# Performance work log

Measured on AMD Instinct MI355X. Metric: run time of the kernel, lower is better.

The kernel has to match this reference:

```python
import jax, jax.numpy as jnp
import numpy as np

NB_CLASSES = 8192
SZ_EMBED = 64
SMOOTHING = 0.1


def setup_inputs() -> dict:
    key = jax.random.key(0)
    k1, k2, k3 = jax.random.split(key, 3)
    X = jax.random.normal(k1, (8192, SZ_EMBED), dtype=jnp.float32)
    T = jax.random.randint(k2, (8192,), 0, NB_CLASSES)
    proxies = jax.random.normal(k3, (NB_CLASSES, SZ_EMBED), dtype=jnp.float32) / 8.0
    return {"X": X, "T": T, "proxies": proxies}


def reference(X, T, proxies):
    # L2-normalize and scale by 3 (as in the torch module)
    Xn = 3.0 * X / jnp.linalg.norm(X, axis=-1, keepdims=True)   # [N, E]
    Pn = 3.0 * proxies / jnp.linalg.norm(proxies, axis=-1, keepdims=True)  # [C, E]

    # squared pairwise distances D[i, c] = ||Xn_i - Pn_c||^2, computed once
    x_sq = jnp.sum(Xn * Xn, axis=-1, keepdims=True)             # [N, 1]
    p_sq = jnp.sum(Pn * Pn, axis=-1)                            # [C]
    D = x_sq + p_sq[None, :] - 2.0 * jnp.einsum('ne,ce->nc', Xn, Pn)  # [N, C]

    # out[i, c] = log( exp(D[i, c]) / sum_c' exp(D[i, c']) )
    out = D - jax.nn.logsumexp(D, axis=-1, keepdims=True)       # [N, C]

    # binarize + smooth labels
    nb_classes = proxies.shape[0]
    onehot = T[:, None] == jnp.arange(nb_classes)[None, :]      # [N, C] bool
    Tm = jnp.where(onehot, 1.0 - SMOOTHING, SMOOTHING / (nb_classes - 1)).astype(X.dtype)

    loss = jnp.mean(jnp.sum(-Tm * out, axis=-1))
    return loss
```

## Files before the change

kernel.cpp:

```cpp
#include <hip/hip_runtime.h>
#include <math.h>

#define NR 8192
#define NC 8192
#define EE 64
#define LOG2E   1.4426950408889634f
#define KSCALE  (-2.0f * LOG2E)
#define C18     (18.0f * LOG2E)
#define NSPLIT  32
#define CPS     (NC / NSPLIT)

typedef __attribute__((ext_vector_type(8))) short bf16x8;
typedef __attribute__((ext_vector_type(4))) float f32x4;

__device__ __forceinline__ float bf2f(unsigned short u) {
    unsigned int x = ((unsigned int)u) << 16;
    return __builtin_bit_cast(float, x);
}
__device__ __forceinline__ unsigned short f2bf(float f) {
    unsigned int u = __builtin_bit_cast(unsigned int, f);
    u += 0x7FFFu + ((u >> 16) & 1u);
    return (unsigned short)(u >> 16);
}

__global__ __launch_bounds__(256) void norm_kernel(
    const float* __restrict__ X, const float* __restrict__ P,
    unsigned short* __restrict__ Xb, unsigned short* __restrict__ Xs,
    unsigned short* __restrict__ Pb)
{
    int row  = blockIdx.x * 4 + (threadIdx.x >> 6);
    int lane = threadIdx.x & 63;
    bool isX = row < NR;
    int r = isX ? row : row - NR;
    const float* src = isX ? X : P;
    float v = src[(size_t)r * EE + lane];
    float s = v * v;
    #pragma unroll
    for (int off = 32; off; off >>= 1) s += __shfl_xor(s, off);
    float xn = v * (3.0f * rsqrtf(s));
    if (isX) {
        Xb[(size_t)r * EE + lane] = f2bf(xn);
        Xs[(size_t)r * EE + lane] = f2bf(xn * KSCALE);
    } else {
        Pb[(size_t)r * EE + lane] = f2bf(xn);
    }
}

__global__ __launch_bounds__(256) void colsum_kernel(
    const unsigned short* __restrict__ Pb, float* __restrict__ sumPnPart)
{
    int w = threadIdx.x >> 6, l = threadIdx.x & 63;
    float acc = 0.f;
    int rbase = blockIdx.x * 128 + w * 32;
    for (int i = 0; i < 32; ++i)
        acc += bf2f(Pb[(size_t)(rbase + i) * EE + l]);
    __shared__ float red[4][64];
    red[w][l] = acc;
    __syncthreads();
    if (w == 0)
        sumPnPart[blockIdx.x * 64 + l] =
            red[0][l] + red[1][l] + red[2][l] + red[3][l];
}

__global__ __launch_bounds__(256) void main_kernel(
    const unsigned short* __restrict__ Xs, const unsigned short* __restrict__ Pb,
    float* __restrict__ ePart)
{
    const int tid = threadIdx.x;
    const int w  = tid >> 6, l = tid & 63;
    const int lr = l & 15, lg = l >> 4;
    const int r0 = blockIdx.x * 256 + w * 64;
    const int cbase = blockIdx.y * CPS;
    const int s = blockIdx.y;

    bf16x8 a[4][2];
    #pragma unroll
    for (int rt = 0; rt < 4; ++rt)
        #pragma unroll
        for (int kk = 0; kk < 2; ++kk)
            a[rt][kk] = *reinterpret_cast<const bf16x8*>(
                Xs + (size_t)(r0 + rt * 16 + lr) * EE + kk * 32 + lg * 8);

    float accE[4][4] = {};
    const f32x4 dinit = {C18, C18, C18, C18};

    #pragma unroll 2
    for (int j = 0; j < CPS / 16; ++j) {
        const int c0 = cbase + j * 16;
        const size_t bb = (size_t)(c0 + lr) * EE + lg * 8;
        bf16x8 b0 = *reinterpret_cast<const bf16x8*>(Pb + bb);
        bf16x8 b1 = *reinterpret_cast<const bf16x8*>(Pb + bb + 32);
        #pragma unroll
        for (int rt = 0; rt < 4; ++rt) {
            f32x4 d = dinit;
            d = __builtin_amdgcn_mfma_f32_16x16x32_bf16(a[rt][0], b0, d, 0, 0, 0);
            d = __builtin_amdgcn_mfma_f32_16x16x32_bf16(a[rt][1], b1, d, 0, 0, 0);
            #pragma unroll
            for (int q = 0; q < 4; ++q)
                accE[rt][q] += __builtin_exp2f(d[q]);
        }
    }

    #pragma unroll
    for (int rt = 0; rt < 4; ++rt)
        #pragma unroll
        for (int q = 0; q < 4; ++q) {
            float v = accE[rt][q];
            v += __shfl_xor(v, 1);
            v += __shfl_xor(v, 2);
            v += __shfl_xor(v, 4);
            v += __shfl_xor(v, 8);
            if (lr == 0)
                ePart[(size_t)(r0 + rt * 16 + lg * 4 + q) * NSPLIT + s] = v;
        }
}

__global__ __launch_bounds__(1024) void final_kernel(
    const unsigned short* __restrict__ Xb, const unsigned short* __restrict__ Pb,
    const int* __restrict__ T, const float* __restrict__ sumPnPart,
    const float* __restrict__ ePart, float* __restrict__ lossPart)
{
    __shared__ float spn[64];
    __shared__ float terms[16];
    int wid = threadIdx.x >> 6, lane = threadIdx.x & 63;

    if (threadIdx.x < 64) {
        float s = 0.f;
        for (int b = 0; b < 64; ++b) s += sumPnPart[b * 64 + threadIdx.x];
        spn[threadIdx.x] = s;
    }
    __syncthreads();

    float sp = spn[lane];
    float wsum = 0.f;
    #pragma unroll
    for (int rr = 0; rr < 4; ++rr) {
        int row = blockIdx.x * 64 + wid * 4 + rr;
        int t = T[row];
        float x  = bf2f(Xb[(size_t)row * EE + lane]);
        float pt = bf2f(Pb[(size_t)t  * EE + lane]);
        float d1 = x * pt;
        float d2 = x * sp;
        float es = (lane < NSPLIT) ? ePart[(size_t)row * NSPLIT + lane] : 0.f;
        #pragma unroll
        for (int off = 32; off; off >>= 1) {
            d1 += __shfl_xor(d1, off);
            d2 += __shfl_xor(d2, off);
            es += __shfl_xor(es, off);
        }
        if (lane == 0) {
            float Dt   = 18.0f - 2.0f * d1;
            float sumD = (float)NC * 18.0f - 2.0f * d2;
            float lse  = __logf(es);
            wsum += lse - (0.9f * Dt + (0.1f / 8191.0f) * (sumD - Dt));
        }
    }
    if (lane == 0) terms[wid] = wsum;
    __syncthreads();
    if (threadIdx.x == 0) {
        float s = 0.f;
        #pragma unroll
        for (int i = 0; i < 16; ++i) s += terms[i];
        lossPart[blockIdx.x] = s;
    }
}

__global__ __launch_bounds__(128) void reduce_kernel(
    const float* __restrict__ lossPart, float* __restrict__ out)
{
    __shared__ float red[2];
    int w = threadIdx.x >> 6, l = threadIdx.x & 63;
    float v = lossPart[threadIdx.x];
    #pragma unroll
    for (int off = 32; off; off >>= 1) v += __shfl_xor(v, off);
    if (l == 0) red[w] = v;
    __syncthreads();
    if (threadIdx.x == 0)
        out[0] = (red[0] + red[1]) * (1.0f / (float)NR);
}

extern "C" void kernel_launch(void* const* d_in, const int* in_sizes, int n_in,
                              void* d_out, int out_size, void* d_ws, size_t ws_size,
                              hipStream_t stream)
{
    const float* X = (const float*)d_in[0];
    const int*   T = (const int*)d_in[1];
    const float* P = (const float*)d_in[2];

    unsigned short* Xb = (unsigned short*)d_ws;
    unsigned short* Xs = Xb + (size_t)NR * EE;
    unsigned short* Pb = Xs + (size_t)NR * EE;
    float* ePart     = (float*)(Pb + (size_t)NC * EE);
    float* sumPnPart = ePart + (size_t)NR * NSPLIT;
    float* lossPart  = sumPnPart + 64 * 64;
    float* out       = (float*)d_out;

    norm_kernel<<<(NR + NC) / 4, 256, 0, stream>>>(X, P, Xb, Xs, Pb);
    colsum_kernel<<<64, 256, 0, stream>>>(Pb, sumPnPart);
    main_kernel<<<dim3(NR / 256, NSPLIT), 256, 0, stream>>>(Xs, Pb, ePart);
    final_kernel<<<NR / 64, 1024, 0, stream>>>(Xb, Pb, T, sumPnPart, ePart, lossPart);
    reduce_kernel<<<1, 128, 0, stream>>>(lossPart, out);
}
```

Baseline: 47.96 us.

## Fold row-sum of distances into main kernel and fuse final reduction via ticket

The main MFMA loop now also accumulates the raw log2-scaled distances alongside the exp sums, so the separate proxy column-sum kernel and the Xb buffer are dropped. The final kernel recovers the sum of distances and target distance from the scaled Xs values. The last block reduces the per-block losses itself, using an atomic ticket that the norm kernel resets, which removes the standalone reduce launch. Two kernel launches and one workspace write are removed. The cost is extra adds in the hot loop and the bf16-scaled Xs being used for the target dot product.

```diff
diff --git a/kernel.cpp b/kernel.cpp
--- a/kernel.cpp
+++ b/kernel.cpp
@@ -5,6 +5,7 @@
 #define NC 8192
 #define EE 64
 #define LOG2E   1.4426950408889634f
+#define LN2     0.6931471805599453f
 #define KSCALE  (-2.0f * LOG2E)
 #define C18     (18.0f * LOG2E)
 #define NSPLIT  32
@@ -25,9 +26,10 @@
 
 __global__ __launch_bounds__(256) void norm_kernel(
     const float* __restrict__ X, const float* __restrict__ P,
-    unsigned short* __restrict__ Xb, unsigned short* __restrict__ Xs,
-    unsigned short* __restrict__ Pb)
+    unsigned short* __restrict__ Xs, unsigned short* __restrict__ Pb,
+    int* __restrict__ ticket)
 {
+    if (blockIdx.x == 0 && threadIdx.x == 0) *ticket = 0;
     int row  = blockIdx.x * 4 + (threadIdx.x >> 6);
     int lane = threadIdx.x & 63;
     bool isX = row < NR;
@@ -38,33 +40,15 @@
     #pragma unroll
     for (int off = 32; off; off >>= 1) s += __shfl_xor(s, off);
     float xn = v * (3.0f * rsqrtf(s));
-    if (isX) {
-        Xb[(size_t)r * EE + lane] = f2bf(xn);
+    if (isX)
         Xs[(size_t)r * EE + lane] = f2bf(xn * KSCALE);
-    } else {
+    else
         Pb[(size_t)r * EE + lane] = f2bf(xn);
-    }
-}
-
-__global__ __launch_bounds__(256) void colsum_kernel(
-    const unsigned short* __restrict__ Pb, float* __restrict__ sumPnPart)
-{
-    int w = threadIdx.x >> 6, l = threadIdx.x & 63;
-    float acc = 0.f;
-    int rbase = blockIdx.x * 128 + w * 32;
-    for (int i = 0; i < 32; ++i)
-        acc += bf2f(Pb[(size_t)(rbase + i) * EE + l]);
-    __shared__ float red[4][64];
-    red[w][l] = acc;
-    __syncthreads();
-    if (w == 0)
-        sumPnPart[blockIdx.x * 64 + l] =
-            red[0][l] + red[1][l] + red[2][l] + red[3][l];
 }
 
 __global__ __launch_bounds__(256) void main_kernel(
     const unsigned short* __restrict__ Xs, const unsigned short* __restrict__ Pb,
-    float* __restrict__ ePart)
+    float* __restrict__ part)
 {
     const int tid = threadIdx.x;
     const int w  = tid >> 6, l = tid & 63;
@@ -82,6 +66,7 @@
                 Xs + (size_t)(r0 + rt * 16 + lr) * EE + kk * 32 + lg * 8);
 
     float accE[4][4] = {};
+    float accD[4][4] = {};
     const f32x4 dinit = {C18, C18, C18, C18};
 
     #pragma unroll 2
@@ -96,8 +81,10 @@
             d = __builtin_amdgcn_mfma_f32_16x16x32_bf16(a[rt][0], b0, d, 0, 0, 0);
             d = __builtin_amdgcn_mfma_f32_16x16x32_bf16(a[rt][1], b1, d, 0, 0, 0);
             #pragma unroll
-            for (int q = 0; q < 4; ++q)
+            for (int q = 0; q < 4; ++q) {
                 accE[rt][q] += __builtin_exp2f(d[q]);
+                accD[rt][q] += d[q];
+            }
         }
     }
 
@@ -105,52 +92,52 @@
     for (int rt = 0; rt < 4; ++rt)
         #pragma unroll
         for (int q = 0; q < 4; ++q) {
-            float v = accE[rt][q];
-            v += __shfl_xor(v, 1);
-            v += __shfl_xor(v, 2);
-            v += __shfl_xor(v, 4);
-            v += __shfl_xor(v, 8);
-            if (lr == 0)
-                ePart[(size_t)(r0 + rt * 16 + lg * 4 + q) * NSPLIT + s] = v;
+            float ve = accE[rt][q];
+            float vd = accD[rt][q];
+            ve += __shfl_xor(ve, 1);  vd += __shfl_xor(vd, 1);
+            ve += __shfl_xor(ve, 2);  vd += __shfl_xor(vd, 2);
+            ve += __shfl_xor(ve, 4);  vd += __shfl_xor(vd, 4);
+            ve += __shfl_xor(ve, 8);  vd += __shfl_xor(vd, 8);
+            if (lr == 0) {
+                const size_t row = r0 + rt * 16 + lg * 4 + q;
+                part[row * 64 + s]      = ve;
+                part[row * 64 + 32 + s] = vd;
+            }
         }
 }
 
 __global__ __launch_bounds__(1024) void final_kernel(
-    const unsigned short* __restrict__ Xb, const unsigned short* __restrict__ Pb,
-    const int* __restrict__ T, const float* __restrict__ sumPnPart,
-    const float* __restrict__ ePart, float* __restrict__ lossPart)
+    const unsigned short* __restrict__ Xs, const unsigned short* __restrict__ Pb,
+    const int* __restrict__ T, const float* __restrict__ part,
+    float* __restrict__ lossPart, int* __restrict__ ticket,
+    float* __restrict__ out)
 {
-    __shared__ float spn[64];
     __shared__ float terms[16];
+    __shared__ int   isLast;
+    __shared__ float red2[2];
     int wid = threadIdx.x >> 6, lane = threadIdx.x & 63;
 
-    if (threadIdx.x < 64) {
-        float s = 0.f;
-        for (int b = 0; b < 64; ++b) s += sumPnPart[b * 64 + threadIdx.x];
-        spn[threadIdx.x] = s;
-    }
-    __syncthreads();
-
-    float sp = spn[lane];
     float wsum = 0.f;
     #pragma unroll
     for (int rr = 0; rr < 4; ++rr) {
         int row = blockIdx.x * 64 + wid * 4 + rr;
         int t = T[row];
-        float x  = bf2f(Xb[(size_t)row * EE + lane]);
+        float xs = bf2f(Xs[(size_t)row * EE + lane]);
         float pt = bf2f(Pb[(size_t)t  * EE + lane]);
-        float d1 = x * pt;
-        float d2 = x * sp;
-        float es = (lane < NSPLIT) ? ePart[(size_t)row * NSPLIT + lane] : 0.f;
+        float d1 = xs * pt;
+        float pv = part[(size_t)row * 64 + lane];
         #pragma unroll
-        for (int off = 32; off; off >>= 1) {
+        for (int off = 1; off <= 16; off <<= 1) {
             d1 += __shfl_xor(d1, off);
-            d2 += __shfl_xor(d2, off);
-            es += __shfl_xor(es, off);
+            pv += __shfl_xor(pv, off);
         }
+        d1 += __shfl_xor(d1, 32);
+        float other = __shfl_xor(pv, 32);
         if (lane == 0) {
-            float Dt   = 18.0f - 2.0f * d1;
-            float sumD = (float)NC * 18.0f - 2.0f * d2;
+            float es   = pv;
+            float ds   = other;
+            float Dt   = 18.0f + d1 * LN2;
+            float sumD = ds * LN2;
             float lse  = __logf(es);
             wsum += lse - (0.9f * Dt + (0.1f / 8191.0f) * (sumD - Dt));
         }
@@ -158,25 +145,26 @@
     if (lane == 0) terms[wid] = wsum;
     __syncthreads();
     if (threadIdx.x == 0) {
-        float s = 0.f;
+        float sB = 0.f;
         #pragma unroll
-        for (int i = 0; i < 16; ++i) s += terms[i];
-        lossPart[blockIdx.x] = s;
+        for (int i = 0; i < 16; ++i) sB += terms[i];
+        lossPart[blockIdx.x] = sB;
+        __threadfence();
+        int old = atomicAdd(ticket, 1);
+        isLast = (old == 127) ? 1 : 0;
     }
-}
-
-__global__ __launch_bounds__(128) void reduce_kernel(
-    const float* __restrict__ lossPart, float* __restrict__ out)
-{
-    __shared__ float red[2];
-    int w = threadIdx.x >> 6, l = threadIdx.x & 63;
-    float v = lossPart[threadIdx.x];
-    #pragma unroll
-    for (int off = 32; off; off >>= 1) v += __shfl_xor(v, off);
-    if (l == 0) red[w] = v;
     __syncthreads();
-    if (threadIdx.x == 0)
-        out[0] = (red[0] + red[1]) * (1.0f / (float)NR);
+    if (isLast) {
+        if (threadIdx.x < 128) {
+            float v = atomicAdd((float*)&lossPart[threadIdx.x], 0.0f);
+            #pragma unroll
+            for (int off = 32; off; off >>= 1) v += __shfl_xor(v, off);
+            if ((threadIdx.x & 63) == 0) red2[threadIdx.x >> 6] = v;
+        }
+        __syncthreads();
+        if (threadIdx.x == 0)
+            out[0] = (red2[0] + red2[1]) * (1.0f / (float)NR);
+    }
 }
 
 extern "C" void kernel_launch(void* const* d_in, const int* in_sizes, int n_in,
@@ -187,17 +175,14 @@
     const int*   T = (const int*)d_in[1];
     const float* P = (const float*)d_in[2];
 
-    unsigned short* Xb = (unsigned short*)d_ws;
-    unsigned short* Xs = Xb + (size_t)NR * EE;
+    unsigned short* Xs = (unsigned short*)d_ws;
     unsigned short* Pb = Xs + (size_t)NR * EE;
-    float* ePart     = (float*)(Pb + (size_t)NC * EE);
-    float* sumPnPart = ePart + (size_t)NR * NSPLIT;
-    float* lossPart  = sumPnPart + 64 * 64;
-    float* out       = (float*)d_out;
+    float* part     = (float*)(Pb + (size_t)NC * EE);
+    float* lossPart = part + (size_t)NR * 64;
+    int*   ticket   = (int*)(lossPart + 128);
+    float* out      = (float*)d_out;
 
-    norm_kernel<<<(NR + NC) / 4, 256, 0, stream>>>(X, P, Xb, Xs, Pb);
-    colsum_kernel<<<64, 256, 0, stream>>>(Pb, sumPnPart);
-    main_kernel<<<dim3(NR / 256, NSPLIT), 256, 0, stream>>>(Xs, Pb, ePart);
-    final_kernel<<<NR / 64, 1024, 0, stream>>>(Xb, Pb, T, sumPnPart, ePart, lossPart);
-    reduce_kernel<<<1, 128, 0, stream>>>(lossPart, out);
+    norm_kernel<<<(NR + NC) / 4, 256, 0, stream>>>(X, P, Xs, Pb, ticket);
+    main_kernel<<<dim3(NR / 256, NSPLIT), 256, 0, stream>>>(Xs, Pb, part);
+    final_kernel<<<NR / 64, 1024, 0, stream>>>(Xs, Pb, T, part, lossPart, ticket, out);
 }
```

New measurement: 48.10 us. Within noise of the previous version (+0.3%).
